# Performance work log

Hardware: AMD Instinct MI355X
Metric: run time of the kernel (lower is better)

## Reference

```python
import jax, jax.numpy as jnp
import numpy as np

D = 128      # entity_and_theorem_embedding_size
M = 8192     # nodes per tree level
L = 5        # internal (non-leaf) levels
V = 4096     # number of input entities (leaf vocab)
K = 8        # number of binary numerical functions
KL = 4       # number of binary logic functions
G = 4096     # number of ground-truth logic statements


def setup_inputs() -> dict:
    key = jax.random.key(0)
    ks = jax.random.split(key, 16)
    s = 0.05
    return {
        "leaf_ids": jax.random.randint(ks[0], (M,), 0, V, dtype=jnp.int32),
        "left_idx": jax.random.randint(ks[1], (L, M), 0, M, dtype=jnp.int32),
        "right_idx": jax.random.randint(ks[2], (L, M), 0, M, dtype=jnp.int32),
        "nf_fid": jax.random.randint(ks[3], (L, M), 0, K, dtype=jnp.int32),
        "gt_left": jax.random.randint(ks[4], (G,), 0, M, dtype=jnp.int32),
        "gt_right": jax.random.randint(ks[5], (G,), 0, M, dtype=jnp.int32),
        "lf_fid": jax.random.randint(ks[6], (G,), 0, KL, dtype=jnp.int32),
        "emb": jax.random.normal(ks[7], (V, D), jnp.float32),
        "W1": jax.random.normal(ks[8], (K, 2 * D, 4 * D), jnp.float32) * s,
        "b1": jnp.zeros((K, 4 * D), jnp.float32),
        "W2": jax.random.normal(ks[9], (K, 4 * D, 2 * D), jnp.float32) * s,
        "b2": jnp.zeros((K, 2 * D), jnp.float32),
        "W3": jax.random.normal(ks[10], (K, 2 * D, D), jnp.float32) * s,
        "b3": jnp.zeros((K, D), jnp.float32),
        "Wl1": jax.random.normal(ks[11], (KL, 2 * D, 4 * D), jnp.float32) * s,
        "bl1": jnp.zeros((KL, 4 * D), jnp.float32),
        "Wl2": jax.random.normal(ks[12], (KL, 4 * D, D), jnp.float32) * s,
        "bl2": jnp.zeros((KL, D), jnp.float32),
    }


def _select(y, fid):
    # y: [N, K, F], fid: [N] -> [N, F]  (per-node dynamic MLP dispatch)
    return jnp.take_along_axis(y, fid[:, None, None], axis=1)[:, 0, :]


def reference(leaf_ids, left_idx, right_idx, nf_fid, gt_left, gt_right, lf_fid,
              emb, W1, b1, W2, b2, W3, b3, Wl1, bl1, Wl2, bl2):
    # Leaf entities: embedding lookup (input_entity_embedding)
    h0 = emb[leaf_ids]  # [M, D]

    # Internal entity nodes: recursive nf_two2one MLPs, level-synchronous
    def level(h, xs):
        li, ri, fid = xs
        x = jnp.concatenate([h[li], h[ri]], axis=-1)          # [M, 2D] concat of operands
        a1 = jax.nn.relu(jnp.einsum('nd,kdf->nkf', x, W1) + b1)   # [M, K, 4D]
        a2 = jax.nn.relu(jnp.einsum('nkd,kdf->nkf', a1, W2) + b2) # [M, K, 2D]
        a3 = jnp.einsum('nkd,kdf->nkf', a2, W3) + b3              # [M, K, D]
        return _select(a3, fid), None
    hL, _ = jax.lax.scan(level, h0, (left_idx, right_idx, nf_fid))

    # Logic statements: lf_two2one MLP on pairs of entity encodings
    xg = jnp.concatenate([hL[gt_left], hL[gt_right]], axis=-1)    # [G, 2D]
    g1 = jax.nn.relu(jnp.einsum('nd,kdf->nkf', xg, Wl1) + bl1)    # [G, KL, 4D]
    g2 = jnp.einsum('nkd,kdf->nkf', g1, Wl2) + bl2                # [G, KL, D]
    return _select(g2, lf_fid)                                    # [G, D]
```

## Files before the change

### kernel.cpp

```cpp
#include <hip/hip_runtime.h>

constexpr int D  = 128;
constexpr int M  = 8192;
constexpr int L  = 5;
constexpr int K  = 8;
constexpr int KL = 4;
constexpr int G  = 4096;

constexpr int TB   = 64;
constexpr int PADL = M + K * TB;
constexpr int PADG = G + KL * TB;

typedef short bf16x8 __attribute__((ext_vector_type(8)));
typedef float f32x4  __attribute__((ext_vector_type(4)));

__device__ __forceinline__ unsigned short f2bf(float x) {
  union { float f; unsigned int u; } c; c.f = x;
  unsigned int u = c.u + 0x7FFF + ((c.u >> 16) & 1);
  return (unsigned short)(u >> 16);
}
__device__ __forceinline__ float bf2f(unsigned short h) {
  union { unsigned int u; float f; } c; c.u = ((unsigned int)h) << 16;
  return c.f;
}

__device__ __forceinline__ int xcd_swizzle(int b, int n) {
  int q = n >> 3, r = n & 7, xcd = b & 7, off = b >> 3;
  return (xcd < r ? xcd * (q + 1) : r * (q + 1) + (xcd - r) * q) + off;
}

__global__ void leaf_gather_kernel(const int* __restrict__ leaf_ids,
                                   const float* __restrict__ emb,
                                   short* __restrict__ hs) {
  int idx = blockIdx.x * 256 + threadIdx.x;
  int n = idx >> 7, d = idx & 127;
  float w = emb[(size_t)leaf_ids[n] * D + d];
  unsigned short hh = f2bf(w);
  hs[n * 256 + d]       = (short)hh;
  hs[n * 256 + 128 + d] = (short)f2bf(w - bf2f(hh));
}

__global__ void bucket64_kernel(const int* __restrict__ nf_fid,
                                const int* __restrict__ lf_fid,
                                int* __restrict__ orders) {
  int b = blockIdx.x;
  const int* fid; int N, Kf, cap; int* out;
  if (b < L) { fid = nf_fid + b * M; N = M; Kf = K;  cap = PADL; out = orders + b * PADL; }
  else       { fid = lf_fid;         N = G; Kf = KL; cap = PADG; out = orders + L * PADL; }
  __shared__ int cnt[8];
  __shared__ int cur[8];
  int tid = threadIdx.x;
  if (tid < Kf) cnt[tid] = 0;
  __syncthreads();
  for (int i = tid; i < N; i += 256) atomicAdd(&cnt[fid[i]], 1);
  __syncthreads();
  if (tid == 0) {
    int off = 0;
    for (int k = 0; k < Kf; ++k) { cur[k] = off; off += ((cnt[k] + TB - 1) / TB) * TB; }
  }
  __syncthreads();
  for (int i = tid; i < cap; i += 256) out[i] = -1;
  __syncthreads();
  for (int i = tid; i < N; i += 256) {
    int kk = fid[i];
    int pos = atomicAdd(&cur[kk], 1);
    out[pos] = i;
  }
}

__global__ void prep_kernel(const float* __restrict__ W1, const float* __restrict__ W2,
                            const float* __restrict__ W3, const float* __restrict__ Wl1,
                            const float* __restrict__ Wl2,
                            short* __restrict__ B1T, short* __restrict__ B2T,
                            short* __restrict__ B3T, short* __restrict__ BL1T,
                            short* __restrict__ BL2T) {
  int b = blockIdx.x;
  const float* W; short* BT; int KD, F;
  if      (b < 256) { W = W1;  BT = B1T;  KD = 256; F = 512; }
  else if (b < 512) { W = W2;  BT = B2T;  KD = 512; F = 256; b -= 256; }
  else if (b < 576) { W = W3;  BT = B3T;  KD = 256; F = 128; b -= 512; }
  else if (b < 704) { W = Wl1; BT = BL1T; KD = 256; F = 512; b -= 576; }
  else              { W = Wl2; BT = BL2T; KD = 512; F = 128; b -= 704; }
  const int ntd = KD >> 6, ntf = F >> 6;
  const int k  = b / (ntd * ntf), rem = b % (ntd * ntf);
  const int d0 = (rem / ntf) << 6, f0 = (rem % ntf) << 6;
  __shared__ float T[64][65];
  const int tid = threadIdx.x;
  const int ln = tid & 63, w4 = tid >> 6;
  #pragma unroll
  for (int i = 0; i < 16; ++i) {
    int d = w4 * 16 + i;
    T[ln][d] = W[((size_t)k * KD + d0 + d) * F + f0 + ln];
  }
  __syncthreads();
  #pragma unroll
  for (int i = 0; i < 16; ++i) {
    int f = w4 * 16 + i;
    float w = T[f][ln];
    unsigned short hi = f2bf(w);
    unsigned short lo = f2bf(w - bf2f(hi));
    size_t base = ((size_t)k * F + f0 + f) * (2 * KD) + d0;
    BT[base + ln]      = (short)hi;
    BT[base + KD + ln] = (short)lo;
  }
}

template<int KH, int NN, int EPI, int FUSED, int TROWS>
__global__ __launch_bounds__(256, TROWS == 64 ? 2 : 3) void mfma_gemm(
    const short* __restrict__ A, const short* __restrict__ hsrc,
    const int* __restrict__ gl, const int* __restrict__ gr,
    const short* __restrict__ BT, const float* __restrict__ bias,
    short* __restrict__ Aout, float* __restrict__ outp,
    const int* __restrict__ order, const int* __restrict__ fid) {
  constexpr int BK    = 64;
  constexpr int NCH   = 3 * KH / BK;
  constexpr int LDA   = BK + 8;
  constexpr int RF    = TROWS / 32;
  constexpr int TPR   = 256 / TROWS;
  __shared__ __align__(16) short As[2][TROWS * LDA];
  __shared__ __align__(16) short Bs[2][128 * LDA];
  __shared__ int nodesS[TROWS], liS[TROWS], riS[TROWS];

  const int tid  = threadIdx.x;
  const int bx   = xcd_swizzle(blockIdx.x, gridDim.x);
  const int row0 = bx * TROWS;
  const int ct   = blockIdx.y;

  if (tid < TROWS) {
    int node = order[row0 + tid];
    nodesS[tid] = node;
    if (FUSED) {
      liS[tid] = node >= 0 ? gl[node] : 0;
      riS[tid] = node >= 0 ? gr[node] : 0;
    }
  }
  __syncthreads();
  if (nodesS[0] < 0) return;
  const int kfn = fid[nodesS[0]];
  const short* __restrict__ Bk = BT + (size_t)kfn * NN * (2 * KH);

  const int lane = tid & 63, wave = tid >> 6;
  const int wr = (wave >> 1) * (TROWS / 2);
  const int wc = wave & 1;
  const int l15 = lane & 15, oct = lane >> 4;

  const int ar = tid / TPR;
  const int ag = (tid % TPR) * (BK / TPR);
  const int bn = tid >> 1;
  const int bg = (tid & 1) * 32;

  f32x4 acc[RF][4];
  #pragma unroll
  for (int i = 0; i < RF; ++i)
    #pragma unroll
    for (int j = 0; j < 4; ++j) acc[i][j] = (f32x4)0.f;

  auto loadB_to = [&](int c, int4& r0, int4& r1, int4& r2, int4& r3) {
    int ko = c * BK, seg = ko / KH, wi = ko % KH;
    int pb = (seg == 2) ? KH + wi : wi;
    const int4* p = (const int4*)(Bk + (size_t)(ct * 128 + bn) * (2 * KH) + pb + bg);
    r0 = p[0]; r1 = p[1]; r2 = p[2]; r3 = p[3];
  };
  auto loadA_to = [&](int c, int4& r0, int4& r1) {
    int ko = c * BK, seg = ko / KH, wi = ko % KH;
    int pa = ((seg == 1) ? KH : 0) + wi + ag;
    if (FUSED) {
      int s4 = pa >> 7;
      int node = (s4 & 1) ? riS[ar] : liS[ar];
      if (nodesS[ar] >= 0) {
        const int4* p = (const int4*)(hsrc + (size_t)node * 256 + ((s4 >> 1) << 7) + (pa & 127));
        r0 = p[0];
        if (TPR == 4) r1 = p[1];
      } else {
        r0 = make_int4(0, 0, 0, 0);
        if (TPR == 4) r1 = make_int4(0, 0, 0, 0);
      }
    } else {
      const int4* p = (const int4*)(A + (size_t)(row0 + ar) * (2 * KH) + pa);
      r0 = p[0];
      if (TPR == 4) r1 = p[1];
    }
  };
  auto storeA = [&](int b, const int4& r0, const int4& r1) {
    int4* d4 = (int4*)&As[b][ar * LDA + ag];
    d4[0] = r0;
    if (TPR == 4) d4[1] = r1;
  };
  auto storeB = [&](int b, const int4& r0, const int4& r1, const int4& r2, const int4& r3) {
    int4* db = (int4*)&Bs[b][bn * LDA + bg];
    db[0] = r0; db[1] = r1; db[2] = r2; db[3] = r3;
  };
  auto compute = [&](int b) {
    __builtin_amdgcn_s_setprio(1);
    #pragma unroll
    for (int s = 0; s < 2; ++s) {
      const int ko = s * 32 + oct * 8;
      bf16x8 afr[RF];
      #pragma unroll
      for (int rf = 0; rf < RF; ++rf)
        afr[rf] = *(const bf16x8*)&As[b][(wr + rf * 16 + l15) * LDA + ko];
      #pragma unroll
      for (int cf = 0; cf < 4; ++cf) {
        bf16x8 bb = *(const bf16x8*)&Bs[b][(wc * 64 + cf * 16 + l15) * LDA + ko];
        #pragma unroll
        for (int rf = 0; rf < RF; ++rf)
          acc[rf][cf] = __builtin_amdgcn_mfma_f32_16x16x32_bf16(afr[rf], bb, acc[rf][cf], 0, 0, 0);
      }
    }
    __builtin_amdgcn_s_setprio(0);
  };
  auto lds_barrier = [&]() {
    asm volatile("s_waitcnt lgkmcnt(0)\n\ts_barrier" ::: "memory");
  };

  int4 a00, a01, a10, a11;
  int4 b00, b01, b02, b03, b10, b11, b12, b13;
  loadA_to(0, a00, a01); loadB_to(0, b00, b01, b02, b03);
  loadA_to(1, a10, a11); loadB_to(1, b10, b11, b12, b13);
  storeA(0, a00, a01); storeB(0, b00, b01, b02, b03);
  lds_barrier();
  for (int c = 0; c < NCH; c += 2) {
    storeA(1, a10, a11); storeB(1, b10, b11, b12, b13);
    if (c + 2 < NCH) { loadA_to(c + 2, a00, a01); loadB_to(c + 2, b00, b01, b02, b03); }
    compute(0);
    lds_barrier();
    if (c + 3 < NCH) { loadA_to(c + 3, a10, a11); loadB_to(c + 3, b10, b11, b12, b13); }
    if (c + 2 < NCH) { storeA(0, a00, a01); storeB(0, b00, b01, b02, b03); }
    compute(1);
    lds_barrier();
  }

  if (EPI == 0) {
    short* Ls = (short*)&Bs[0][0];
    #pragma unroll
    for (int part = 0; part < 2; ++part) {
      __syncthreads();
      #pragma unroll
      for (int rf = 0; rf < RF; ++rf)
        #pragma unroll
        for (int cf = 0; cf < 4; ++cf) {
          int colL = wc * 64 + cf * 16 + l15;
          float bv = bias[kfn * NN + ct * 128 + colL];
          #pragma unroll
          for (int j = 0; j < 4; ++j) {
            int row = wr + rf * 16 + oct * 4 + j;
            float v = fmaxf(acc[rf][cf][j] + bv, 0.f);
            unsigned short hh = f2bf(v);
            unsigned short val = (part == 0) ? hh : f2bf(v - bf2f(hh));
            Ls[row * 128 + colL] = (short)val;
          }
        }
      __syncthreads();
      constexpr int SPT = TROWS / 2;
      constexpr int TPW = 128 / SPT;
      int row = tid / TPW, sg = (tid % TPW) * SPT;
      const int4* src = (const int4*)&Ls[row * 128 + sg];
      int4* dst = (int4*)&Aout[(size_t)(row0 + row) * (2 * NN) + part * NN + ct * 128 + sg];
      #pragma unroll
      for (int q = 0; q < SPT / 8; ++q) dst[q] = src[q];
    }
  } else if (EPI == 1) {
    float* Lf = (float*)&Bs[0][0];
    #pragma unroll
    for (int h = 0; h < 2; ++h) {
      __syncthreads();
      if (wc == h) {
        #pragma unroll
        for (int rf = 0; rf < RF; ++rf)
          #pragma unroll
          for (int cf = 0; cf < 4; ++cf) {
            int colL = cf * 16 + l15;
            float bv = bias[kfn * 128 + h * 64 + colL];
            #pragma unroll
            for (int j = 0; j < 4; ++j) {
              int row = wr + rf * 16 + oct * 4 + j;
              Lf[row * 64 + colL] = acc[rf][cf][j] + bv;
            }
          }
      }
      __syncthreads();
      constexpr int FPT = TROWS / 4;
      constexpr int TPW = 64 / FPT;
      int row = tid / TPW, off = (tid % TPW) * FPT;
      int node = nodesS[row];
      if (node >= 0) {
        const float4* src = (const float4*)&Lf[row * 64 + off];
        float4* dst = (float4*)&outp[(size_t)node * 128 + h * 64 + off];
        #pragma unroll
        for (int q = 0; q < FPT / 4; ++q) dst[q] = src[q];
      }
    }
  } else {
    short* Ls = (short*)&Bs[0][0];
    #pragma unroll
    for (int rf = 0; rf < RF; ++rf)
      #pragma unroll
      for (int cf = 0; cf < 4; ++cf) {
        int colL = wc * 64 + cf * 16 + l15;
        float bv = bias[kfn * 128 + colL];
        #pragma unroll
        for (int j = 0; j < 4; ++j) {
          int row = wr + rf * 16 + oct * 4 + j;
          float v = acc[rf][cf][j] + bv;
          unsigned short hh = f2bf(v);
          Ls[row * 256 + colL]       = (short)hh;
          Ls[row * 256 + 128 + colL] = (short)f2bf(v - bf2f(hh));
        }
      }
    __syncthreads();
    constexpr int SPT = TROWS;
    constexpr int TPW = 256 / SPT;
    int row = tid / TPW, sg = (tid % TPW) * SPT;
    int node = nodesS[row];
    if (node >= 0) {
      const int4* src = (const int4*)&Ls[row * 256 + sg];
      int4* dst = (int4*)&Aout[(size_t)node * 256 + sg];
      #pragma unroll
      for (int q = 0; q < SPT / 8; ++q) dst[q] = src[q];
    }
  }
}

extern "C" void kernel_launch(void* const* d_in, const int* in_sizes, int n_in,
                              void* d_out, int out_size, void* d_ws, size_t ws_size,
                              hipStream_t stream) {
  const int*   leaf_ids  = (const int*)d_in[0];
  const int*   left_idx  = (const int*)d_in[1];
  const int*   right_idx = (const int*)d_in[2];
  const int*   nf_fid    = (const int*)d_in[3];
  const int*   gt_left   = (const int*)d_in[4];
  const int*   gt_right  = (const int*)d_in[5];
  const int*   lf_fid    = (const int*)d_in[6];
  const float* emb       = (const float*)d_in[7];
  const float* W1 = (const float*)d_in[8];
  const float* b1 = (const float*)d_in[9];
  const float* W2 = (const float*)d_in[10];
  const float* b2 = (const float*)d_in[11];
  const float* W3 = (const float*)d_in[12];
  const float* b3 = (const float*)d_in[13];
  const float* Wl1 = (const float*)d_in[14];
  const float* bl1 = (const float*)d_in[15];
  const float* Wl2 = (const float*)d_in[16];
  const float* bl2 = (const float*)d_in[17];
  float* out = (float*)d_out;

  const size_t SZ_H    = (size_t)M * 256 * 2;
  const size_t SZ_A1   = (size_t)PADL * 1024 * 2;
  const size_t SZ_A2   = (size_t)PADL * 512 * 2;
  const size_t SZ_B1T  = (size_t)8 * 512 * 512 * 2;
  const size_t SZ_B2T  = (size_t)8 * 256 * 1024 * 2;
  const size_t SZ_B3T  = (size_t)8 * 128 * 512 * 2;
  const size_t SZ_BL1T = (size_t)4 * 512 * 512 * 2;
  const size_t SZ_BL2T = (size_t)4 * 128 * 1024 * 2;

  char* p = (char*)d_ws;
  short* hsA  = (short*)p;  p += SZ_H;
  short* hsB  = (short*)p;  p += SZ_H;
  short* a1s  = (short*)p;  p += SZ_A1;
  short* a2s  = (short*)p;  p += SZ_A2;
  short* B1T  = (short*)p;  p += SZ_B1T;
  short* B2T  = (short*)p;  p += SZ_B2T;
  short* B3T  = (short*)p;  p += SZ_B3T;
  short* BL1T = (short*)p;  p += SZ_BL1T;
  short* BL2T = (short*)p;  p += SZ_BL2T;
  int*   orders = (int*)p;

  leaf_gather_kernel<<<(M * D) / 256, 256, 0, stream>>>(leaf_ids, emb, hsA);
  bucket64_kernel<<<L + 1, 256, 0, stream>>>(nf_fid, lf_fid, orders);
  prep_kernel<<<768, 256, 0, stream>>>(W1, W2, W3, Wl1, Wl2,
                                       B1T, B2T, B3T, BL1T, BL2T);

  short* hin = hsA;
  short* hout = hsB;
  for (int l = 0; l < L; ++l) {
    const int* ord = orders + l * PADL;
    const int* fidl = nf_fid + l * M;
    mfma_gemm<256, 512, 0, 1, 64><<<dim3(PADL / 64, 4), 256, 0, stream>>>(
        nullptr, hin, left_idx + l * M, right_idx + l * M,
        B1T, b1, a1s, nullptr, ord, fidl);
    mfma_gemm<512, 256, 0, 0, 64><<<dim3(PADL / 64, 2), 256, 0, stream>>>(
        a1s, nullptr, nullptr, nullptr,
        B2T, b2, a2s, nullptr, ord, fidl);
    mfma_gemm<256, 128, 2, 0, 32><<<dim3(PADL / 32, 1), 256, 0, stream>>>(
        a2s, nullptr, nullptr, nullptr,
        B3T, b3, hout, nullptr, ord, fidl);
    short* t = hin; hin = hout; hout = t;
  }
  const int* ordG = orders + L * PADL;
  mfma_gemm<256, 512, 0, 1, 64><<<dim3(PADG / 64, 4), 256, 0, stream>>>(
      nullptr, hin, gt_left, gt_right,
      BL1T, bl1, a1s, nullptr, ordG, lf_fid);
  mfma_gemm<512, 128, 1, 0, 32><<<dim3(PADG / 32, 1), 256, 0, stream>>>(
      a1s, nullptr, nullptr, nullptr,
      BL2T, bl2, nullptr, out, ordG, lf_fid);
}
```

Baseline: 500.7 us.

## Fuse all stages into one persistent cooperative kernel with grid syncs

Replaces the roughly twenty separate launches (leaf gather, bucketing, weight prep, per-level GEMMs, logic MLP) with one persistent cooperative kernel. It loops over tiles per stage and uses grid-wide syncs between dependent stages, with the old multi-launch path kept as a fallback. The aim is to remove launch overhead and tail gaps between the many small kernels. In exchange it adds grid-sync cost, drops the XCD swizzle, and the fixed grid (capped at 512 blocks) can leave some stages imbalanced, e.g. 544 tiles over 512 blocks. The inline LDS barrier asm is also replaced with __syncthreads, and the order of a store and prefetch is swapped.

```diff
diff --git a/kernel.cpp b/kernel.cpp
--- a/kernel.cpp
+++ b/kernel.cpp
@@ -1,4 +1,7 @@
 #include <hip/hip_runtime.h>
+#include <hip/hip_cooperative_groups.h>
+
+namespace cg = cooperative_groups;
 
 constexpr int D  = 128;
 constexpr int M  = 8192;
@@ -29,64 +32,35 @@
   return (xcd < r ? xcd * (q + 1) : r * (q + 1) + (xcd - r) * q) + off;
 }
 
-__global__ void leaf_gather_kernel(const int* __restrict__ leaf_ids,
-                                   const float* __restrict__ emb,
-                                   short* __restrict__ hs) {
-  int idx = blockIdx.x * 256 + threadIdx.x;
+struct P {
+  const int *leaf_ids, *left_idx, *right_idx, *nf_fid, *gt_left, *gt_right, *lf_fid;
+  const float *emb, *W1, *b1, *W2, *b2, *W3, *b3, *Wl1, *bl1, *Wl2, *bl2;
+  float* out;
+  short *hsA, *hsB, *a1s, *a2s, *B1T, *B2T, *B3T, *BL1T, *BL2T;
+  int* orders;
+};
+
+__device__ __forceinline__ void leaf_unit(int u, const P& p) {
+  int idx = u * 256 + threadIdx.x;
   int n = idx >> 7, d = idx & 127;
-  float w = emb[(size_t)leaf_ids[n] * D + d];
+  float w = p.emb[(size_t)p.leaf_ids[n] * D + d];
   unsigned short hh = f2bf(w);
-  hs[n * 256 + d]       = (short)hh;
-  hs[n * 256 + 128 + d] = (short)f2bf(w - bf2f(hh));
-}
-
-__global__ void bucket64_kernel(const int* __restrict__ nf_fid,
-                                const int* __restrict__ lf_fid,
-                                int* __restrict__ orders) {
-  int b = blockIdx.x;
-  const int* fid; int N, Kf, cap; int* out;
-  if (b < L) { fid = nf_fid + b * M; N = M; Kf = K;  cap = PADL; out = orders + b * PADL; }
-  else       { fid = lf_fid;         N = G; Kf = KL; cap = PADG; out = orders + L * PADL; }
-  __shared__ int cnt[8];
-  __shared__ int cur[8];
-  int tid = threadIdx.x;
-  if (tid < Kf) cnt[tid] = 0;
-  __syncthreads();
-  for (int i = tid; i < N; i += 256) atomicAdd(&cnt[fid[i]], 1);
-  __syncthreads();
-  if (tid == 0) {
-    int off = 0;
-    for (int k = 0; k < Kf; ++k) { cur[k] = off; off += ((cnt[k] + TB - 1) / TB) * TB; }
-  }
-  __syncthreads();
-  for (int i = tid; i < cap; i += 256) out[i] = -1;
-  __syncthreads();
-  for (int i = tid; i < N; i += 256) {
-    int kk = fid[i];
-    int pos = atomicAdd(&cur[kk], 1);
-    out[pos] = i;
-  }
-}
-
-__global__ void prep_kernel(const float* __restrict__ W1, const float* __restrict__ W2,
-                            const float* __restrict__ W3, const float* __restrict__ Wl1,
-                            const float* __restrict__ Wl2,
-                            short* __restrict__ B1T, short* __restrict__ B2T,
-                            short* __restrict__ B3T, short* __restrict__ BL1T,
-                            short* __restrict__ BL2T) {
-  int b = blockIdx.x;
+  p.hsA[n * 256 + d]       = (short)hh;
+  p.hsA[n * 256 + 128 + d] = (short)f2bf(w - bf2f(hh));
+}
+
+__device__ void prep_tile(int b, const P& p, float (*T)[65]) {
   const float* W; short* BT; int KD, F;
-  if      (b < 256) { W = W1;  BT = B1T;  KD = 256; F = 512; }
-  else if (b < 512) { W = W2;  BT = B2T;  KD = 512; F = 256; b -= 256; }
-  else if (b < 576) { W = W3;  BT = B3T;  KD = 256; F = 128; b -= 512; }
-  else if (b < 704) { W = Wl1; BT = BL1T; KD = 256; F = 512; b -= 576; }
-  else              { W = Wl2; BT = BL2T; KD = 512; F = 128; b -= 704; }
+  if      (b < 256) { W = p.W1;  BT = p.B1T;  KD = 256; F = 512; }
+  else if (b < 512) { W = p.W2;  BT = p.B2T;  KD = 512; F = 256; b -= 256; }
+  else if (b < 576) { W = p.W3;  BT = p.B3T;  KD = 256; F = 128; b -= 512; }
+  else if (b < 704) { W = p.Wl1; BT = p.BL1T; KD = 256; F = 512; b -= 576; }
+  else              { W = p.Wl2; BT = p.BL2T; KD = 512; F = 128; b -= 704; }
   const int ntd = KD >> 6, ntf = F >> 6;
   const int k  = b / (ntd * ntf), rem = b % (ntd * ntf);
   const int d0 = (rem / ntf) << 6, f0 = (rem % ntf) << 6;
-  __shared__ float T[64][65];
-  const int tid = threadIdx.x;
-  const int ln = tid & 63, w4 = tid >> 6;
+  const int tid = threadIdx.x, ln = tid & 63, w4 = tid >> 6;
+  __syncthreads();
   #pragma unroll
   for (int i = 0; i < 16; ++i) {
     int d = w4 * 16 + i;
@@ -105,27 +79,50 @@
   }
 }
 
+__device__ void bucket_body(int b, const P& p, int* cnt, int* cur) {
+  const int* fid; int N, Kf, cap; int* outp;
+  if (b < L) { fid = p.nf_fid + b * M; N = M; Kf = K;  cap = PADL; outp = p.orders + b * PADL; }
+  else       { fid = p.lf_fid;         N = G; Kf = KL; cap = PADG; outp = p.orders + L * PADL; }
+  int tid = threadIdx.x;
+  if (tid < Kf) cnt[tid] = 0;
+  __syncthreads();
+  for (int i = tid; i < N; i += 256) atomicAdd(&cnt[fid[i]], 1);
+  __syncthreads();
+  if (tid == 0) {
+    int off = 0;
+    for (int k = 0; k < Kf; ++k) { cur[k] = off; off += ((cnt[k] + TB - 1) / TB) * TB; }
+  }
+  __syncthreads();
+  for (int i = tid; i < cap; i += 256) outp[i] = -1;
+  __syncthreads();
+  for (int i = tid; i < N; i += 256) {
+    int kk = fid[i];
+    int pos = atomicAdd(&cur[kk], 1);
+    outp[pos] = i;
+  }
+}
+
 template<int KH, int NN, int EPI, int FUSED, int TROWS>
-__global__ __launch_bounds__(256, TROWS == 64 ? 2 : 3) void mfma_gemm(
+__device__ void gemm_tile(
+    int bx, int ct,
     const short* __restrict__ A, const short* __restrict__ hsrc,
     const int* __restrict__ gl, const int* __restrict__ gr,
     const short* __restrict__ BT, const float* __restrict__ bias,
     short* __restrict__ Aout, float* __restrict__ outp,
-    const int* __restrict__ order, const int* __restrict__ fid) {
-  constexpr int BK    = 64;
-  constexpr int NCH   = 3 * KH / BK;
-  constexpr int LDA   = BK + 8;
-  constexpr int RF    = TROWS / 32;
-  constexpr int TPR   = 256 / TROWS;
-  __shared__ __align__(16) short As[2][TROWS * LDA];
-  __shared__ __align__(16) short Bs[2][128 * LDA];
-  __shared__ int nodesS[TROWS], liS[TROWS], riS[TROWS];
+    const int* __restrict__ order, const int* __restrict__ fid,
+    short* As, short* Bs, int* nodesS, int* liS, int* riS) {
+  constexpr int BK   = 64;
+  constexpr int NCH  = 3 * KH / BK;
+  constexpr int LDA  = 72;
+  constexpr int ASTR = TROWS * LDA;
+  constexpr int BSTR = 128 * LDA;
+  constexpr int RF   = TROWS / 32;
+  constexpr int TPR  = 256 / TROWS;
 
   const int tid  = threadIdx.x;
-  const int bx   = xcd_swizzle(blockIdx.x, gridDim.x);
   const int row0 = bx * TROWS;
-  const int ct   = blockIdx.y;
-
+
+  __syncthreads();
   if (tid < TROWS) {
     int node = order[row0 + tid];
     nodesS[tid] = node;
@@ -158,8 +155,8 @@
   auto loadB_to = [&](int c, int4& r0, int4& r1, int4& r2, int4& r3) {
     int ko = c * BK, seg = ko / KH, wi = ko % KH;
     int pb = (seg == 2) ? KH + wi : wi;
-    const int4* p = (const int4*)(Bk + (size_t)(ct * 128 + bn) * (2 * KH) + pb + bg);
-    r0 = p[0]; r1 = p[1]; r2 = p[2]; r3 = p[3];
+    const int4* q = (const int4*)(Bk + (size_t)(ct * 128 + bn) * (2 * KH) + pb + bg);
+    r0 = q[0]; r1 = q[1]; r2 = q[2]; r3 = q[3];
   };
   auto loadA_to = [&](int c, int4& r0, int4& r1) {
     int ko = c * BK, seg = ko / KH, wi = ko % KH;
@@ -168,26 +165,26 @@
       int s4 = pa >> 7;
       int node = (s4 & 1) ? riS[ar] : liS[ar];
       if (nodesS[ar] >= 0) {
-        const int4* p = (const int4*)(hsrc + (size_t)node * 256 + ((s4 >> 1) << 7) + (pa & 127));
-        r0 = p[0];
-        if (TPR == 4) r1 = p[1];
+        const int4* q = (const int4*)(hsrc + (size_t)node * 256 + ((s4 >> 1) << 7) + (pa & 127));
+        r0 = q[0];
+        if (TPR == 4) r1 = q[1];
       } else {
         r0 = make_int4(0, 0, 0, 0);
         if (TPR == 4) r1 = make_int4(0, 0, 0, 0);
       }
     } else {
-      const int4* p = (const int4*)(A + (size_t)(row0 + ar) * (2 * KH) + pa);
-      r0 = p[0];
-      if (TPR == 4) r1 = p[1];
+      const int4* q = (const int4*)(A + (size_t)(row0 + ar) * (2 * KH) + pa);
+      r0 = q[0];
+      if (TPR == 4) r1 = q[1];
     }
   };
   auto storeA = [&](int b, const int4& r0, const int4& r1) {
-    int4* d4 = (int4*)&As[b][ar * LDA + ag];
+    int4* d4 = (int4*)&As[b * ASTR + ar * LDA + ag];
     d4[0] = r0;
     if (TPR == 4) d4[1] = r1;
   };
   auto storeB = [&](int b, const int4& r0, const int4& r1, const int4& r2, const int4& r3) {
-    int4* db = (int4*)&Bs[b][bn * LDA + bg];
+    int4* db = (int4*)&Bs[b * BSTR + bn * LDA + bg];
     db[0] = r0; db[1] = r1; db[2] = r2; db[3] = r3;
   };
   auto compute = [&](int b) {
@@ -198,19 +195,16 @@
       bf16x8 afr[RF];
       #pragma unroll
       for (int rf = 0; rf < RF; ++rf)
-        afr[rf] = *(const bf16x8*)&As[b][(wr + rf * 16 + l15) * LDA + ko];
+        afr[rf] = *(const bf16x8*)&As[b * ASTR + (wr + rf * 16 + l15) * LDA + ko];
       #pragma unroll
       for (int cf = 0; cf < 4; ++cf) {
-        bf16x8 bb = *(const bf16x8*)&Bs[b][(wc * 64 + cf * 16 + l15) * LDA + ko];
+        bf16x8 bb = *(const bf16x8*)&Bs[b * BSTR + (wc * 64 + cf * 16 + l15) * LDA + ko];
         #pragma unroll
         for (int rf = 0; rf < RF; ++rf)
           acc[rf][cf] = __builtin_amdgcn_mfma_f32_16x16x32_bf16(afr[rf], bb, acc[rf][cf], 0, 0, 0);
       }
     }
     __builtin_amdgcn_s_setprio(0);
-  };
-  auto lds_barrier = [&]() {
-    asm volatile("s_waitcnt lgkmcnt(0)\n\ts_barrier" ::: "memory");
   };
 
   int4 a00, a01, a10, a11;
@@ -218,20 +212,20 @@
   loadA_to(0, a00, a01); loadB_to(0, b00, b01, b02, b03);
   loadA_to(1, a10, a11); loadB_to(1, b10, b11, b12, b13);
   storeA(0, a00, a01); storeB(0, b00, b01, b02, b03);
-  lds_barrier();
+  __syncthreads();
   for (int c = 0; c < NCH; c += 2) {
     storeA(1, a10, a11); storeB(1, b10, b11, b12, b13);
     if (c + 2 < NCH) { loadA_to(c + 2, a00, a01); loadB_to(c + 2, b00, b01, b02, b03); }
     compute(0);
-    lds_barrier();
+    __syncthreads();
+    if (c + 2 < NCH) { storeA(0, a00, a01); storeB(0, b00, b01, b02, b03); }
     if (c + 3 < NCH) { loadA_to(c + 3, a10, a11); loadB_to(c + 3, b10, b11, b12, b13); }
-    if (c + 2 < NCH) { storeA(0, a00, a01); storeB(0, b00, b01, b02, b03); }
     compute(1);
-    lds_barrier();
+    __syncthreads();
   }
 
   if (EPI == 0) {
-    short* Ls = (short*)&Bs[0][0];
+    short* Ls = Bs;
     #pragma unroll
     for (int part = 0; part < 2; ++part) {
       __syncthreads();
@@ -260,7 +254,7 @@
       for (int q = 0; q < SPT / 8; ++q) dst[q] = src[q];
     }
   } else if (EPI == 1) {
-    float* Lf = (float*)&Bs[0][0];
+    float* Lf = (float*)Bs;
     #pragma unroll
     for (int h = 0; h < 2; ++h) {
       __syncthreads();
@@ -291,7 +285,7 @@
       }
     }
   } else {
-    short* Ls = (short*)&Bs[0][0];
+    short* Ls = Bs;
     #pragma unroll
     for (int rf = 0; rf < RF; ++rf)
       #pragma unroll
@@ -321,6 +315,81 @@
   }
 }
 
+__global__ __launch_bounds__(256, 2) void mega(P p) {
+  __shared__ __align__(16) short As[2 * 64 * 72];
+  __shared__ __align__(16) short Bs[2 * 128 * 72];
+  __shared__ int nodesS[64], liS[64], riS[64];
+  __shared__ int cnt[8], cur[8];
+
+  cg::grid_group grid = cg::this_grid();
+  const int bid = blockIdx.x;
+  const int NB  = gridDim.x;
+
+  for (int u = bid; u < (M * D) / 256; u += NB) leaf_unit(u, p);
+  {
+    float (*T)[65] = reinterpret_cast<float (*)[65]>(&Bs[0]);
+    for (int t = bid; t < 768; t += NB) prep_tile(t, p, T);
+  }
+  if (bid < L + 1) bucket_body(bid, p, cnt, cur);
+  __threadfence();
+  grid.sync();
+
+  short* hin  = p.hsA;
+  short* hout = p.hsB;
+  for (int l = 0; l < L; ++l) {
+    const int* ord = p.orders + l * PADL;
+    const int* fl  = p.nf_fid + l * M;
+    for (int t = bid; t < 544; t += NB)
+      gemm_tile<256, 512, 0, 1, 64>(t % 136, t / 136, nullptr, hin,
+          p.left_idx + l * M, p.right_idx + l * M, p.B1T, p.b1,
+          p.a1s, nullptr, ord, fl, As, Bs, nodesS, liS, riS);
+    __threadfence(); grid.sync();
+    for (int t = bid; t < 272; t += NB)
+      gemm_tile<512, 256, 0, 0, 64>(t % 136, t / 136, p.a1s, nullptr,
+          nullptr, nullptr, p.B2T, p.b2,
+          p.a2s, nullptr, ord, fl, As, Bs, nodesS, liS, riS);
+    __threadfence(); grid.sync();
+    for (int t = bid; t < 272; t += NB)
+      gemm_tile<256, 128, 2, 0, 32>(t, 0, p.a2s, nullptr,
+          nullptr, nullptr, p.B3T, p.b3,
+          hout, nullptr, ord, fl, As, Bs, nodesS, liS, riS);
+    __threadfence(); grid.sync();
+    short* tmp = hin; hin = hout; hout = tmp;
+  }
+  const int* ordG = p.orders + L * PADL;
+  for (int t = bid; t < 272; t += NB)
+    gemm_tile<256, 512, 0, 1, 64>(t % 68, t / 68, nullptr, hin,
+        p.gt_left, p.gt_right, p.BL1T, p.bl1,
+        p.a1s, nullptr, ordG, p.lf_fid, As, Bs, nodesS, liS, riS);
+  __threadfence(); grid.sync();
+  for (int t = bid; t < 136; t += NB)
+    gemm_tile<512, 128, 1, 0, 32>(t, 0, p.a1s, nullptr,
+        nullptr, nullptr, p.BL2T, p.bl2,
+        nullptr, p.out, ordG, p.lf_fid, As, Bs, nodesS, liS, riS);
+}
+
+__global__ void leaf_k(P p) { leaf_unit(blockIdx.x, p); }
+__global__ void bucket_k(P p) {
+  __shared__ int cnt[8], cur[8];
+  bucket_body(blockIdx.x, p, cnt, cur);
+}
+__global__ void prep_k(P p) {
+  __shared__ float T[64][65];
+  prep_tile(blockIdx.x, p, T);
+}
+template<int KH, int NN, int EPI, int FUSED, int TROWS>
+__global__ __launch_bounds__(256, TROWS == 64 ? 2 : 3) void gemm_k(
+    const short* A, const short* hsrc, const int* gl, const int* gr,
+    const short* BT, const float* bias, short* Aout, float* outp,
+    const int* order, const int* fid) {
+  __shared__ __align__(16) short As[2 * TROWS * 72];
+  __shared__ __align__(16) short Bs[2 * 128 * 72];
+  __shared__ int nodesS[TROWS], liS[TROWS], riS[TROWS];
+  int bx = xcd_swizzle(blockIdx.x, gridDim.x);
+  gemm_tile<KH, NN, EPI, FUSED, TROWS>(bx, blockIdx.y, A, hsrc, gl, gr, BT,
+      bias, Aout, outp, order, fid, As, Bs, nodesS, liS, riS);
+}
+
 extern "C" void kernel_launch(void* const* d_in, const int* in_sizes, int n_in,
                               void* d_out, int out_size, void* d_ws, size_t ws_size,
                               hipStream_t stream) {
@@ -332,17 +401,6 @@
   const int*   gt_right  = (const int*)d_in[5];
   const int*   lf_fid    = (const int*)d_in[6];
   const float* emb       = (const float*)d_in[7];
-  const float* W1 = (const float*)d_in[8];
-  const float* b1 = (const float*)d_in[9];
-  const float* W2 = (const float*)d_in[10];
-  const float* b2 = (const float*)d_in[11];
-  const float* W3 = (const float*)d_in[12];
-  const float* b3 = (const float*)d_in[13];
-  const float* Wl1 = (const float*)d_in[14];
-  const float* bl1 = (const float*)d_in[15];
-  const float* Wl2 = (const float*)d_in[16];
-  const float* bl2 = (const float*)d_in[17];
-  float* out = (float*)d_out;
 
   const size_t SZ_H    = (size_t)M * 256 * 2;
   const size_t SZ_A1   = (size_t)PADL * 1024 * 2;
@@ -353,44 +411,60 @@
   const size_t SZ_BL1T = (size_t)4 * 512 * 512 * 2;
   const size_t SZ_BL2T = (size_t)4 * 128 * 1024 * 2;
 
-  char* p = (char*)d_ws;
-  short* hsA  = (short*)p;  p += SZ_H;
-  short* hsB  = (short*)p;  p += SZ_H;
-  short* a1s  = (short*)p;  p += SZ_A1;
-  short* a2s  = (short*)p;  p += SZ_A2;
-  short* B1T  = (short*)p;  p += SZ_B1T;
-  short* B2T  = (short*)p;  p += SZ_B2T;
-  short* B3T  = (short*)p;  p += SZ_B3T;
-  short* BL1T = (short*)p;  p += SZ_BL1T;
-  short* BL2T = (short*)p;  p += SZ_BL2T;
-  int*   orders = (int*)p;
-
-  leaf_gather_kernel<<<(M * D) / 256, 256, 0, stream>>>(leaf_ids, emb, hsA);
-  bucket64_kernel<<<L + 1, 256, 0, stream>>>(nf_fid, lf_fid, orders);
-  prep_kernel<<<768, 256, 0, stream>>>(W1, W2, W3, Wl1, Wl2,
-                                       B1T, B2T, B3T, BL1T, BL2T);
-
+  char* q = (char*)d_ws;
+  short* hsA  = (short*)q;  q += SZ_H;
+  short* hsB  = (short*)q;  q += SZ_H;
+  short* a1s  = (short*)q;  q += SZ_A1;
+  short* a2s  = (short*)q;  q += SZ_A2;
+  short* B1T  = (short*)q;  q += SZ_B1T;
+  short* B2T  = (short*)q;  q += SZ_B2T;
+  short* B3T  = (short*)q;  q += SZ_B3T;
+  short* BL1T = (short*)q;  q += SZ_BL1T;
+  short* BL2T = (short*)q;  q += SZ_BL2T;
+  int*   orders = (int*)q;
+
+  P prm;
+  prm.leaf_ids = leaf_ids; prm.left_idx = left_idx; prm.right_idx = right_idx;
+  prm.nf_fid = nf_fid; prm.gt_left = gt_left; prm.gt_right = gt_right;
+  prm.lf_fid = lf_fid; prm.emb = emb;
+  prm.W1 = (const float*)d_in[8];  prm.b1 = (const float*)d_in[9];
+  prm.W2 = (const float*)d_in[10]; prm.b2 = (const float*)d_in[11];
+  prm.W3 = (const float*)d_in[12]; prm.b3 = (const float*)d_in[13];
+  prm.Wl1 = (const float*)d_in[14]; prm.bl1 = (const float*)d_in[15];
+  prm.Wl2 = (const float*)d_in[16]; prm.bl2 = (const float*)d_in[17];
+  prm.out = (float*)d_out;
+  prm.hsA = hsA; prm.hsB = hsB; prm.a1s = a1s; prm.a2s = a2s;
+  prm.B1T = B1T; prm.B2T = B2T; prm.B3T = B3T; prm.BL1T = BL1T; prm.BL2T = BL2T;
+  prm.orders = orders;
+
+  int maxB = 0;
+  hipError_t oe = hipOccupancyMaxActiveBlocksPerMultiprocessor(&maxB, mega, 256, 0);
+  int grid = (oe == hipSuccess && maxB >= 1) ? maxB * 256 : 256;
+  if (grid > 512) grid = 512;
+  void* args[] = { (void*)&prm };
+  hipError_t e = hipLaunchCooperativeKernel(mega, dim3(grid), dim3(256), args, 0, stream);
+  if (e == hipSuccess) return;
+
+  leaf_k<<<(M * D) / 256, 256, 0, stream>>>(prm);
+  bucket_k<<<L + 1, 256, 0, stream>>>(prm);
+  prep_k<<<768, 256, 0, stream>>>(prm);
   short* hin = hsA;
   short* hout = hsB;
   for (int l = 0; l < L; ++l) {
     const int* ord = orders + l * PADL;
-    const int* fidl = nf_fid + l * M;
-    mfma_gemm<256, 512, 0, 1, 64><<<dim3(PADL / 64, 4), 256, 0, stream>>>(
+    const int* fl  = nf_fid + l * M;
+    gemm_k<256, 512, 0, 1, 64><<<dim3(PADL / 64, 4), 256, 0, stream>>>(
         nullptr, hin, left_idx + l * M, right_idx + l * M,
-        B1T, b1, a1s, nullptr, ord, fidl);
-    mfma_gemm<512, 256, 0, 0, 64><<<dim3(PADL / 64, 2), 256, 0, stream>>>(
-        a1s, nullptr, nullptr, nullptr,
-        B2T, b2, a2s, nullptr, ord, fidl);
-    mfma_gemm<256, 128, 2, 0, 32><<<dim3(PADL / 32, 1), 256, 0, stream>>>(
-        a2s, nullptr, nullptr, nullptr,
-        B3T, b3, hout, nullptr, ord, fidl);
+        B1T, prm.b1, a1s, nullptr, ord, fl);
+    gemm_k<512, 256, 0, 0, 64><<<dim3(PADL / 64, 2), 256, 0, stream>>>(
+        a1s, nullptr, nullptr, nullptr, B2T, prm.b2, a2s, nullptr, ord, fl);
+    gemm_k<256, 128, 2, 0, 32><<<dim3(PADL / 32, 1), 256, 0, stream>>>(
+        a2s, nullptr, nullptr, nullptr, B3T, prm.b3, hout, nullptr, ord, fl);
     short* t = hin; hin = hout; hout = t;
   }
   const int* ordG = orders + L * PADL;
-  mfma_gemm<256, 512, 0, 1, 64><<<dim3(PADG / 64, 4), 256, 0, stream>>>(
-      nullptr, hin, gt_left, gt_right,
-      BL1T, bl1, a1s, nullptr, ordG, lf_fid);
-  mfma_gemm<512, 128, 1, 0, 32><<<dim3(PADG / 32, 1), 256, 0, stream>>>(
-      a1s, nullptr, nullptr, nullptr,
-      BL2T, bl2, nullptr, out, ordG, lf_fid);
-}
+  gemm_k<256, 512, 0, 1, 64><<<dim3(PADG / 64, 4), 256, 0, stream>>>(
+      nullptr, hin, gt_left, gt_right, BL1T, prm.bl1, a1s, nullptr, ordG, lf_fid);
+  gemm_k<512, 128, 1, 0, 32><<<dim3(PADG / 32, 1), 256, 0, stream>>>(
+      a1s, nullptr, nullptr, nullptr, BL2T, prm.bl2, nullptr, prm.out, ordG, lf_fid);
+}
```

Result: slower. 1.561 ms (+211.8%).
